# Optimization experiments

Hardware: AMD Instinct MI355X
Metric: run time of the kernel (lower is better)

The kernel has to match this reference:

```python
import jax, jax.numpy as jnp
import numpy as np

N_NODES = 100000
N_EDGES = 1600000
N_GRAPHS = 1000
NODES_PER_GRAPH = 100  # batch vector is arange(N)//100: exactly 100 nodes per graph
HID = 32
MAX_Z = 1000
K = 30
D_LAT = HID * 3 + 1  # 97, total_latent_dim


def setup_inputs() -> dict:
    key = jax.random.key(0)
    ks = jax.random.split(key, 24)
    s = 1.0 / np.sqrt(HID)
    inp = {
        "z": jax.random.randint(ks[0], (N_NODES,), 0, MAX_Z, dtype=jnp.int32),
        "edge_index": jax.random.randint(ks[1], (2, N_EDGES), 0, N_NODES, dtype=jnp.int32),
        "batch": (jnp.arange(N_NODES, dtype=jnp.int32) // NODES_PER_GRAPH),
        "edge_weight": jax.random.uniform(ks[2], (N_EDGES,), jnp.float32, 0.1, 1.0),
        "z_emb": jax.random.normal(ks[3], (MAX_Z, HID), jnp.float32) * 0.1,
        # GCNConv stack: [32->32, 32->32, 32->32, 32->1]
        "Wg1": jax.random.normal(ks[4], (HID, HID)) * s,
        "bg1": jnp.zeros((HID,), jnp.float32),
        "Wg2": jax.random.normal(ks[5], (HID, HID)) * s,
        "bg2": jnp.zeros((HID,), jnp.float32),
        "Wg3": jax.random.normal(ks[6], (HID, HID)) * s,
        "bg3": jnp.zeros((HID,), jnp.float32),
        "Wg4": jax.random.normal(ks[7], (HID, 1)) * s,
        "bg4": jnp.zeros((1,), jnp.float32),
        # Conv1d(1, 16, kernel=97, stride=97)
        "Wc1": jax.random.normal(ks[8], (16, D_LAT)) * (1.0 / np.sqrt(D_LAT)),
        "bc1": jnp.zeros((16,), jnp.float32),
        # Conv1d(16, 32, kernel=5, stride=1)
        "Wc2": jax.random.normal(ks[9], (32, 16, 5)) * (1.0 / np.sqrt(16 * 5)),
        "bc2": jnp.zeros((32,), jnp.float32),
        # Linear(352, 128), Linear(128, 1)
        "Wl1": jax.random.normal(ks[10], (352, 128)) * (1.0 / np.sqrt(352)),
        "bl1": jnp.zeros((128,), jnp.float32),
        "Wl2": jax.random.normal(ks[11], (128, 1)) * (1.0 / np.sqrt(128)),
        "bl2": jnp.zeros((1,), jnp.float32),
    }
    return inp


def gcn_conv(x, src, dst, ew, W, b, n):
    # PyG GCNConv: xW, add self-loops (weight 1), sym-normalize, aggregate at dst, + bias
    xw = x @ W
    deg = jax.ops.segment_sum(ew, dst, num_segments=n) + 1.0  # +1 for self loop
    dinv = jnp.where(deg > 0, jax.lax.rsqrt(deg), 0.0)
    norm = dinv[src] * ew * dinv[dst]                          # [E]
    out = jax.ops.segment_sum(norm[:, None] * xw[src], dst, num_segments=n)
    out = out + xw * (dinv * dinv)[:, None]                    # self-loop term
    return out + b


def _forward(z, edge_index, batch, edge_weight, z_emb, Wg1, bg1, Wg2, bg2, Wg3, bg3,
             Wg4, bg4, Wc1, bc1, Wc2, bc2, Wl1, bl1, Wl2, bl2):
    src, dst = edge_index[0], edge_index[1]
    n = z.shape[0]
    x = z_emb[z]                                              # [N, 32]
    xs = []
    h = x
    for W, b in ((Wg1, bg1), (Wg2, bg2), (Wg3, bg3), (Wg4, bg4)):
        h = jnp.tanh(gcn_conv(h, src, dst, edge_weight, W, b, n))
        xs.append(h)
    x = jnp.concatenate(xs, axis=-1)                          # [N, 97]
    # global_sort_pool: batch is uniform (100 nodes/graph) so dense batching is a reshape
    dense = x.reshape(N_GRAPHS, NODES_PER_GRAPH, D_LAT)       # [B, 100, 97]
    idx = jnp.argsort(-dense[:, :, -1], axis=1)[:, :K]        # sort desc by last channel
    top = jnp.take_along_axis(dense, idx[:, :, None], axis=1)  # [B, 30, 97]
    # Conv1d(1,16,97,stride=97) on flattened [B,1,30*97] == per-slot dense layer
    y = jax.nn.relu(jnp.einsum('bkd,cd->bck', top, Wc1) + bc1[None, :, None])  # [B,16,30]
    y = y.reshape(N_GRAPHS, 16, K // 2, 2).max(axis=-1)        # MaxPool1d(2,2) -> [B,16,15]
    y = jax.lax.conv_general_dilated(y, Wc2, (1,), 'VALID',
                                     dimension_numbers=('NCH', 'OIH', 'NCH'))
    y = jax.nn.relu(y + bc2[None, :, None])                    # [B,32,11]
    y = y.reshape(N_GRAPHS, -1)                                # [B,352]
    y = jax.nn.relu(y @ Wl1 + bl1)                             # dropout: eval mode, identity
    return y @ Wl2 + bl2                                       # [B,1]


def reference(z, edge_index, batch, edge_weight, z_emb, Wg1, bg1, Wg2, bg2, Wg3, bg3,
              Wg4, bg4, Wc1, bc1, Wc2, bc2, Wl1, bl1, Wl2, bl2):
    return _forward(z, edge_index, batch, edge_weight, z_emb, Wg1, bg1, Wg2, bg2, Wg3,
                    bg3, Wg4, bg4, Wc1, bc1, Wc2, bc2, Wl1, bl1, Wl2, bl2)
```

## Files before the change

### kernel.cpp

```cpp
#include <hip/hip_runtime.h>

#define HID 32
#define DLAT 97
#define NPG 100
#define TOPK 30
#define BKT_NODES 128
#define BKT_SHIFT 7
#define MAXBKT 1024
#define CAP 3072
#define CHUNK 8192


__global__ __launch_bounds__(256) void binA_kernel(const int* __restrict__ dst,
                                                   int* __restrict__ bucket_cnt, int E) {
    __shared__ int hist[MAXBKT];
    for (int t = threadIdx.x; t < MAXBKT; t += 256) hist[t] = 0;
    __syncthreads();
    int base = blockIdx.x * CHUNK;
    int lim = min(E, base + CHUNK);
    for (int e = base + threadIdx.x; e < lim; e += 256)
        atomicAdd(&hist[dst[e] >> BKT_SHIFT], 1);
    __syncthreads();
    for (int t = threadIdx.x; t < MAXBKT; t += 256) {
        int v = hist[t];
        if (v) atomicAdd(&bucket_cnt[t], v);
    }
}

__global__ __launch_bounds__(MAXBKT) void bscan_kernel(const int* __restrict__ bucket_cnt,
                                                       int* __restrict__ bucket_start,
                                                       int* __restrict__ cursor) {
    __shared__ int sh[MAXBKT];
    int t = threadIdx.x;
    int v = bucket_cnt[t];
    sh[t] = v;
    __syncthreads();
    for (int off = 1; off < MAXBKT; off <<= 1) {
        int tv = (t >= off) ? sh[t - off] : 0;
        __syncthreads();
        sh[t] += tv;
        __syncthreads();
    }
    int excl = sh[t] - v;
    bucket_start[t] = excl;
    cursor[t] = excl;
    if (t == MAXBKT - 1) bucket_start[MAXBKT] = sh[t];
}

__global__ __launch_bounds__(256) void binB_kernel(const int* __restrict__ src,
                                                   const int* __restrict__ dst,
                                                   const float* __restrict__ ew,
                                                   int* __restrict__ cursor,
                                                   int2* __restrict__ bedge, int E) {
    __shared__ int hist[MAXBKT];
    __shared__ int lcur[MAXBKT];
    __shared__ int dcache[CHUNK];
    for (int t = threadIdx.x; t < MAXBKT; t += 256) hist[t] = 0;
    __syncthreads();
    int base = blockIdx.x * CHUNK;
    int M = min(E - base, CHUNK);
    for (int i = threadIdx.x; i < M; i += 256) {
        int d = dst[base + i];
        dcache[i] = d;
        atomicAdd(&hist[d >> BKT_SHIFT], 1);
    }
    __syncthreads();
    for (int t = threadIdx.x; t < MAXBKT; t += 256) {
        int v = hist[t];
        lcur[t] = v ? atomicAdd(&cursor[t], v) : 0;
    }
    __syncthreads();
    for (int i = threadIdx.x; i < M; i += 256) {
        int d = dcache[i];
        int slot = atomicAdd(&lcur[d >> BKT_SHIFT], 1);
        bedge[slot] = make_int2(src[base + i] | ((d & (BKT_NODES - 1)) << 20),
                                __float_as_int(ew[base + i]));
    }
}

__global__ __launch_bounds__(256) void sortlocal_kernel(
    const int2* __restrict__ bedge, const int* __restrict__ bucket_start,
    int2* __restrict__ csr, int* __restrict__ row_start, float* __restrict__ dinv,
    int N, int E) {
    __shared__ int2 LDSe[CAP];
    __shared__ int cnt[BKT_NODES];
    __shared__ int sh[BKT_NODES];
    __shared__ int lcur[BKT_NODES];
    __shared__ float facc[BKT_NODES];
    int b = blockIdx.x, t = threadIdx.x;
    int beg = bucket_start[b], end = bucket_start[b + 1], M = end - beg;
    if (t < BKT_NODES) { cnt[t] = 0; facc[t] = 0.f; }
    __syncthreads();
    int n = b * BKT_NODES + t;
    if (M <= CAP) {
        for (int i = t; i < M; i += 256) {
            int2 e = bedge[beg + i];
            LDSe[i] = e;
            atomicAdd(&cnt[(e.x >> 20) & (BKT_NODES - 1)], 1);
        }
        __syncthreads();
        int v = 0;
        if (t < BKT_NODES) { v = cnt[t]; sh[t] = v; }
        __syncthreads();
        for (int off = 1; off < BKT_NODES; off <<= 1) {
            int tv = (t >= off && t < BKT_NODES) ? sh[t - off] : 0;
            __syncthreads();
            if (t < BKT_NODES) sh[t] += tv;
            __syncthreads();
        }
        int excl = 0;
        if (t < BKT_NODES) {
            excl = sh[t] - v;
            lcur[t] = excl;
            if (n < N) row_start[n] = beg + excl;
        }
        if (b == 0 && t == 0) row_start[N] = E;
        __syncthreads();
        for (int i = t; i < M; i += 256) {
            int2 e = LDSe[i];
            int slot = atomicAdd(&lcur[(e.x >> 20) & (BKT_NODES - 1)], 1);
            csr[beg + slot] = make_int2(e.x & 0xFFFFF, e.y);
        }
        __syncthreads();
        if (t < BKT_NODES && n < N) {
            float s = 1.f;
            int s0 = beg + excl;
            for (int i = 0; i < v; ++i) s += __int_as_float(csr[s0 + i].y);
            dinv[n] = 1.f / sqrtf(s);
        }
    } else {
        for (int i = beg + t; i < end; i += 256) {
            int2 e = bedge[i];
            int loc = (e.x >> 20) & (BKT_NODES - 1);
            atomicAdd(&cnt[loc], 1);
            atomicAdd(&facc[loc], __int_as_float(e.y));
        }
        __syncthreads();
        int v = 0;
        if (t < BKT_NODES) { v = cnt[t]; sh[t] = v; }
        __syncthreads();
        for (int off = 1; off < BKT_NODES; off <<= 1) {
            int tv = (t >= off && t < BKT_NODES) ? sh[t - off] : 0;
            __syncthreads();
            if (t < BKT_NODES) sh[t] += tv;
            __syncthreads();
        }
        if (t < BKT_NODES) {
            int excl = sh[t] - v;
            lcur[t] = excl;
            if (n < N) {
                row_start[n] = beg + excl;
                dinv[n] = 1.f / sqrtf(1.f + facc[t]);
            }
        }
        if (b == 0 && t == 0) row_start[N] = E;
        __syncthreads();
        for (int i = beg + t; i < end; i += 256) {
            int2 e = bedge[i];
            int slot = atomicAdd(&lcur[(e.x >> 20) & (BKT_NODES - 1)], 1);
            csr[beg + slot] = make_int2(e.x & 0xFFFFF, e.y);
        }
    }
}

__global__ void xw1_kernel(const int* __restrict__ z, const float* __restrict__ z_emb,
                           const float* __restrict__ W, const float* __restrict__ dinv,
                           float* __restrict__ xw, int N) {
    int tid = blockIdx.x * blockDim.x + threadIdx.x;
    if (tid >= N * HID) return;
    int n = tid >> 5, f = tid & 31;
    const float* row = z_emb + (size_t)z[n] * HID;
    float s = 0.f;
#pragma unroll
    for (int k = 0; k < HID; ++k) s += row[k] * W[k * HID + f];
    xw[tid] = s * dinv[n];
}

template <int MODE>
__global__ __launch_bounds__(256) void agg32f_kernel(
    const int* __restrict__ row_start, const int2* __restrict__ csr,
    const float* __restrict__ xw, const float* __restrict__ b,
    const float* __restrict__ dinv, const float* __restrict__ Wn,
    float* __restrict__ concat, int col_off, float* __restrict__ xw_next, int N) {
    int tid = blockIdx.x * blockDim.x + threadIdx.x;
    int n = tid >> 5;
    if (n >= N) return;
    int f = threadIdx.x & 31;
    int beg = row_start[n], end = row_start[n + 1];
    float s0 = 0.f, s1 = 0.f;
    for (int i = beg; i < end; i += 8) {
        float w[8];
        int idx[8];
#pragma unroll
        for (int j = 0; j < 8; ++j) {
            int ii = min(i + j, end - 1);
            int2 v = csr[ii];
            idx[j] = v.x;
            w[j] = (i + j < end) ? __int_as_float(v.y) : 0.f;
        }
        float x[8];
#pragma unroll
        for (int j = 0; j < 8; ++j) x[j] = xw[(size_t)idx[j] * HID + f];
#pragma unroll
        for (int j = 0; j < 8; ++j) {
            if (j & 1) s1 += w[j] * x[j];
            else       s0 += w[j] * x[j];
        }
    }
    float s = s0 + s1;
    float di = dinv[n];
    float outv = tanhf(di * (s + xw[(size_t)n * HID + f]) + b[f]);
    concat[(size_t)n * DLAT + col_off + f] = outv;

    if (MODE == 0) {
        float p = 0.f;
#pragma unroll
        for (int k = 0; k < HID; ++k) {
            float ok = __shfl(outv, k, 32);
            p += ok * Wn[k * HID + f];
        }
        xw_next[(size_t)n * HID + f] = p * di;
    } else {
        float p = outv * Wn[f];
        p += __shfl_xor(p, 16);
        p += __shfl_xor(p, 8);
        p += __shfl_xor(p, 4);
        p += __shfl_xor(p, 2);
        p += __shfl_xor(p, 1);
        if (f == 0) xw_next[n] = p * di;
    }
}

__global__ __launch_bounds__(128) void topk_head_kernel(
    const int* __restrict__ row_start, const int2* __restrict__ csr,
    const float* __restrict__ xw4, const float* __restrict__ b4,
    const float* __restrict__ dinv, const float* __restrict__ concat,
    const float* __restrict__ Wc1, const float* __restrict__ bc1,
    const float* __restrict__ Wc2, const float* __restrict__ bc2,
    const float* __restrict__ Wl1, const float* __restrict__ bl1,
    const float* __restrict__ Wl2, const float* __restrict__ bl2,
    float* __restrict__ out) {
    int g = blockIdx.x;
    int tid = threadIdx.x;
    __shared__ float v[NPG];
    __shared__ int tidx[TOPK];
    __shared__ float tval[TOPK];
    __shared__ float top[TOPK * DLAT];
    __shared__ float y1[16 * TOPK];
    __shared__ float y2[16 * 15];
    __shared__ float y3[352];
    __shared__ float r[128];

    if (tid < NPG) {
        int n = g * NPG + tid;
        int beg = row_start[n], end = row_start[n + 1];
        float s = 0.f;
        for (int i = beg; i < end; ++i) {
            int2 e = csr[i];
            s += __int_as_float(e.y) * xw4[e.x];
        }
        v[tid] = tanhf(dinv[n] * (s + xw4[n]) + b4[0]);
    }
    __syncthreads();
    if (tid < NPG) {
        float vi = v[tid];
        int cnt = 0;
#pragma unroll 4
        for (int j = 0; j < NPG; ++j) {
            float vj = v[j];
            cnt += (vj > vi) || (vj == vi && j < tid);
        }
        if (cnt < TOPK) {
            tidx[cnt] = g * NPG + tid;
            tval[cnt] = vi;
        }
    }
    __syncthreads();

    for (int idx = tid; idx < TOPK * DLAT; idx += 128) {
        int k = idx / DLAT, d = idx - k * DLAT;
        top[idx] = (d == 96) ? tval[k] : concat[(size_t)tidx[k] * DLAT + d];
    }
    __syncthreads();

    for (int idx = tid; idx < 16 * TOPK; idx += 128) {
        int c = idx / TOPK, k = idx % TOPK;
        float s = bc1[c];
        const float* w = Wc1 + c * DLAT;
        const float* t = top + k * DLAT;
#pragma unroll 4
        for (int d = 0; d < DLAT; ++d) s += t[d] * w[d];
        y1[c * TOPK + k] = fmaxf(s, 0.f);
    }
    __syncthreads();

    for (int idx = tid; idx < 16 * 15; idx += 128) {
        int c = idx / 15, j = idx % 15;
        y2[idx] = fmaxf(y1[c * TOPK + 2 * j], y1[c * TOPK + 2 * j + 1]);
    }
    __syncthreads();

    for (int idx = tid; idx < 352; idx += 128) {
        int o = idx / 11, t = idx % 11;
        float s = bc2[o];
#pragma unroll
        for (int i = 0; i < 16; ++i) {
#pragma unroll
            for (int k = 0; k < 5; ++k)
                s += Wc2[(o * 16 + i) * 5 + k] * y2[i * 15 + t + k];
        }
        y3[idx] = fmaxf(s, 0.f);
    }
    __syncthreads();

    {
        float s = bl1[tid];
        for (int d = 0; d < 352; ++d) s += y3[d] * Wl1[d * 128 + tid];
        r[tid] = fmaxf(s, 0.f) * Wl2[tid];
    }
    __syncthreads();
    if (tid < 64) r[tid] += r[tid + 64];
    __syncthreads();
    if (tid == 0) {
        float s = 0.f;
        for (int j = 0; j < 64; ++j) s += r[j];
        out[g] = s + bl2[0];
    }
}


extern "C" void kernel_launch(void* const* d_in, const int* in_sizes, int n_in,
                              void* d_out, int out_size, void* d_ws, size_t ws_size,
                              hipStream_t stream) {
    const int* z = (const int*)d_in[0];
    const int* ei = (const int*)d_in[1];
    const float* ew = (const float*)d_in[3];
    const float* z_emb = (const float*)d_in[4];
    const float* Wg[4] = {(const float*)d_in[5], (const float*)d_in[7],
                          (const float*)d_in[9], (const float*)d_in[11]};
    const float* bg[4] = {(const float*)d_in[6], (const float*)d_in[8],
                          (const float*)d_in[10], (const float*)d_in[12]};
    const float* Wc1 = (const float*)d_in[13];
    const float* bc1 = (const float*)d_in[14];
    const float* Wc2 = (const float*)d_in[15];
    const float* bc2 = (const float*)d_in[16];
    const float* Wl1 = (const float*)d_in[17];
    const float* bl1 = (const float*)d_in[18];
    const float* Wl2 = (const float*)d_in[19];
    const float* bl2 = (const float*)d_in[20];
    float* out = (float*)d_out;

    const int N = in_sizes[0];
    const int E = in_sizes[1] / 2;
    const int G = out_size;
    const int* src = ei;
    const int* dst = ei + E;

    auto cdiv = [](long long a, long long b) { return (int)((a + b - 1) / b); };
    const int NB = cdiv(E, CHUNK);
    const int NBKT = cdiv(N, BKT_NODES);

    char* ws = (char*)d_ws;
    int2* bedge = (int2*)ws;                  ws += sizeof(int2) * (size_t)E;
    int2* csr = (int2*)ws;                    ws += sizeof(int2) * (size_t)E;
    int* bucket_cnt = (int*)ws;               ws += sizeof(int) * MAXBKT;
    int* bucket_start = (int*)ws;             ws += sizeof(int) * (MAXBKT + 1);
    int* cursor = (int*)ws;                   ws += sizeof(int) * MAXBKT;
    int* row_start = (int*)ws;                ws += sizeof(int) * (N + 1);
    float* dinv = (float*)ws;                 ws += sizeof(float) * N;
    float* xw_a = (float*)ws;                 ws += sizeof(float) * (size_t)N * HID;
    float* concat = (float*)ws;               ws += sizeof(float) * (size_t)N * DLAT;
    float* xw4 = (float*)ws;                  ws += sizeof(float) * N;
    float* xw_b = (float*)bedge;

    const int B = 256;

    hipMemsetAsync(bucket_cnt, 0, sizeof(int) * MAXBKT, stream);
    binA_kernel<<<NB, B, 0, stream>>>(dst, bucket_cnt, E);
    bscan_kernel<<<1, MAXBKT, 0, stream>>>(bucket_cnt, bucket_start, cursor);
    binB_kernel<<<NB, B, 0, stream>>>(src, dst, ew, cursor, bedge, E);
    sortlocal_kernel<<<NBKT, B, 0, stream>>>(bedge, bucket_start, csr, row_start,
                                             dinv, N, E);

    xw1_kernel<<<cdiv((long long)N * HID, B), B, 0, stream>>>(z, z_emb, Wg[0], dinv, xw_a, N);
    const int AGGB = cdiv((long long)N * 32, B);
    agg32f_kernel<0><<<AGGB, B, 0, stream>>>(row_start, csr, xw_a, bg[0], dinv, Wg[1],
                                             concat, 0, xw_b, N);
    agg32f_kernel<0><<<AGGB, B, 0, stream>>>(row_start, csr, xw_b, bg[1], dinv, Wg[2],
                                             concat, 32, xw_a, N);
    agg32f_kernel<1><<<AGGB, B, 0, stream>>>(row_start, csr, xw_a, bg[2], dinv, Wg[3],
                                             concat, 64, xw4, N);

    topk_head_kernel<<<G, 128, 0, stream>>>(row_start, csr, xw4, bg[3], dinv, concat,
                                            Wc1, bc1, Wc2, bc2, Wl1, bl1, Wl2, bl2, out);
}
```

Baseline: 417.5 us.

## Precompute per-atom-type embedding×W table and gather it in first aggregation

```diff
diff --git a/kernel.cpp b/kernel.cpp
--- a/kernel.cpp
+++ b/kernel.cpp
@@ -4,6 +4,7 @@
 #define DLAT 97
 #define NPG 100
 #define TOPK 30
+#define MAXZ 1000
 #define BKT_NODES 128
 #define BKT_SHIFT 7
 #define MAXBKT 1024
@@ -80,8 +81,8 @@
 
 __global__ __launch_bounds__(256) void sortlocal_kernel(
     const int2* __restrict__ bedge, const int* __restrict__ bucket_start,
-    int2* __restrict__ csr, int* __restrict__ row_start, float* __restrict__ dinv,
-    int N, int E) {
+    const int* __restrict__ z, int2* __restrict__ csr, int* __restrict__ row_start,
+    float* __restrict__ dinv, int2* __restrict__ ni, int N, int E) {
     __shared__ int2 LDSe[CAP];
     __shared__ int cnt[BKT_NODES];
     __shared__ int sh[BKT_NODES];
@@ -126,7 +127,9 @@
             float s = 1.f;
             int s0 = beg + excl;
             for (int i = 0; i < v; ++i) s += __int_as_float(csr[s0 + i].y);
-            dinv[n] = 1.f / sqrtf(s);
+            float di = 1.f / sqrtf(s);
+            dinv[n] = di;
+            ni[n] = make_int2(z[n], __float_as_int(di));
         }
     } else {
         for (int i = beg + t; i < end; i += 256) {
@@ -150,7 +153,9 @@
             lcur[t] = excl;
             if (n < N) {
                 row_start[n] = beg + excl;
-                dinv[n] = 1.f / sqrtf(1.f + facc[t]);
+                float di = 1.f / sqrtf(1.f + facc[t]);
+                dinv[n] = di;
+                ni[n] = make_int2(z[n], __float_as_int(di));
             }
         }
         if (b == 0 && t == 0) row_start[N] = E;
@@ -163,17 +168,59 @@
     }
 }
 
-__global__ void xw1_kernel(const int* __restrict__ z, const float* __restrict__ z_emb,
-                           const float* __restrict__ W, const float* __restrict__ dinv,
-                           float* __restrict__ xw, int N) {
+__global__ void ztab_kernel(const float* __restrict__ z_emb, const float* __restrict__ W,
+                            float* __restrict__ T) {
     int tid = blockIdx.x * blockDim.x + threadIdx.x;
-    if (tid >= N * HID) return;
-    int n = tid >> 5, f = tid & 31;
-    const float* row = z_emb + (size_t)z[n] * HID;
+    if (tid >= MAXZ * HID) return;
+    int zi = tid >> 5, f = tid & 31;
+    const float* row = z_emb + (size_t)zi * HID;
     float s = 0.f;
 #pragma unroll
     for (int k = 0; k < HID; ++k) s += row[k] * W[k * HID + f];
-    xw[tid] = s * dinv[n];
+    T[tid] = s;
+}
+
+__global__ __launch_bounds__(256) void agg1st_kernel(
+    const int* __restrict__ row_start, const int2* __restrict__ csr,
+    const int2* __restrict__ ni, const float* __restrict__ T,
+    const float* __restrict__ b, const float* __restrict__ Wn,
+    float* __restrict__ concat, float* __restrict__ xw_next, int N) {
+    int tid = blockIdx.x * blockDim.x + threadIdx.x;
+    int n = tid >> 5;
+    if (n >= N) return;
+    int f = threadIdx.x & 31;
+    int beg = row_start[n], end = row_start[n + 1];
+    float s0 = 0.f, s1 = 0.f;
+    for (int i = beg; i < end; i += 8) {
+        int2 e[8];
+#pragma unroll
+        for (int j = 0; j < 8; ++j) e[j] = csr[min(i + j, end - 1)];
+        int2 nio[8];
+#pragma unroll
+        for (int j = 0; j < 8; ++j) nio[j] = ni[e[j].x];
+        float x[8];
+#pragma unroll
+        for (int j = 0; j < 8; ++j) x[j] = T[nio[j].x * HID + f];
+#pragma unroll
+        for (int j = 0; j < 8; ++j) {
+            float w = (i + j < end)
+                          ? __int_as_float(e[j].y) * __int_as_float(nio[j].y) : 0.f;
+            if (j & 1) s1 += w * x[j];
+            else       s0 += w * x[j];
+        }
+    }
+    float s = s0 + s1;
+    int2 me = ni[n];
+    float di = __int_as_float(me.y);
+    float outv = tanhf(di * (s + di * T[me.x * HID + f]) + b[f]);
+    concat[(size_t)n * DLAT + f] = outv;
+    float p = 0.f;
+#pragma unroll
+    for (int k = 0; k < HID; ++k) {
+        float ok = __shfl(outv, k, 32);
+        p += ok * Wn[k * HID + f];
+    }
+    xw_next[(size_t)n * HID + f] = p * di;
 }
 
 template <int MODE>
@@ -363,15 +410,17 @@
     char* ws = (char*)d_ws;
     int2* bedge = (int2*)ws;                  ws += sizeof(int2) * (size_t)E;
     int2* csr = (int2*)ws;                    ws += sizeof(int2) * (size_t)E;
+    int2* ni = (int2*)ws;                     ws += sizeof(int2) * (size_t)N;
     int* bucket_cnt = (int*)ws;               ws += sizeof(int) * MAXBKT;
     int* bucket_start = (int*)ws;             ws += sizeof(int) * (MAXBKT + 1);
     int* cursor = (int*)ws;                   ws += sizeof(int) * MAXBKT;
     int* row_start = (int*)ws;                ws += sizeof(int) * (N + 1);
     float* dinv = (float*)ws;                 ws += sizeof(float) * N;
+    float* T = (float*)ws;                    ws += sizeof(float) * MAXZ * HID;
     float* xw_a = (float*)ws;                 ws += sizeof(float) * (size_t)N * HID;
     float* concat = (float*)ws;               ws += sizeof(float) * (size_t)N * DLAT;
-    float* xw4 = (float*)ws;                  ws += sizeof(float) * N;
     float* xw_b = (float*)bedge;
+    float* xw4 = (float*)ni;
 
     const int B = 256;
 
@@ -379,13 +428,13 @@
     binA_kernel<<<NB, B, 0, stream>>>(dst, bucket_cnt, E);
     bscan_kernel<<<1, MAXBKT, 0, stream>>>(bucket_cnt, bucket_start, cursor);
     binB_kernel<<<NB, B, 0, stream>>>(src, dst, ew, cursor, bedge, E);
-    sortlocal_kernel<<<NBKT, B, 0, stream>>>(bedge, bucket_start, csr, row_start,
-                                             dinv, N, E);
-
-    xw1_kernel<<<cdiv((long long)N * HID, B), B, 0, stream>>>(z, z_emb, Wg[0], dinv, xw_a, N);
+    sortlocal_kernel<<<NBKT, B, 0, stream>>>(bedge, bucket_start, z, csr, row_start,
+                                             dinv, ni, N, E);
+
+    ztab_kernel<<<cdiv(MAXZ * HID, B), B, 0, stream>>>(z_emb, Wg[0], T);
     const int AGGB = cdiv((long long)N * 32, B);
-    agg32f_kernel<0><<<AGGB, B, 0, stream>>>(row_start, csr, xw_a, bg[0], dinv, Wg[1],
-                                             concat, 0, xw_b, N);
+    agg1st_kernel<<<AGGB, B, 0, stream>>>(row_start, csr, ni, T, bg[0], Wg[1],
+                                          concat, xw_b, N);
     agg32f_kernel<0><<<AGGB, B, 0, stream>>>(row_start, csr, xw_b, bg[1], dinv, Wg[2],
                                              concat, 32, xw_a, N);
     agg32f_kernel<1><<<AGGB, B, 0, stream>>>(row_start, csr, xw_a, bg[2], dinv, Wg[3],
```

Result: no change. 423.6 us (+1.5%).

## Fuse CSR build stages and first projection into one cooperative kernel

Applied to the files above, without the earlier changes.

```diff
diff --git a/kernel.cpp b/kernel.cpp
--- a/kernel.cpp
+++ b/kernel.cpp
@@ -1,4 +1,7 @@
 #include <hip/hip_runtime.h>
+#include <hip/hip_cooperative_groups.h>
+
+namespace cg = cooperative_groups;
 
 #define HID 32
 #define DLAT 97
@@ -6,174 +9,166 @@
 #define TOPK 30
 #define BKT_NODES 128
 #define BKT_SHIFT 7
-#define MAXBKT 1024
+#define NBUCK 1024
 #define CAP 3072
 #define CHUNK 8192
 
-
-__global__ __launch_bounds__(256) void binA_kernel(const int* __restrict__ dst,
-                                                   int* __restrict__ bucket_cnt, int E) {
-    __shared__ int hist[MAXBKT];
-    for (int t = threadIdx.x; t < MAXBKT; t += 256) hist[t] = 0;
-    __syncthreads();
-    int base = blockIdx.x * CHUNK;
-    int lim = min(E, base + CHUNK);
-    for (int e = base + threadIdx.x; e < lim; e += 256)
-        atomicAdd(&hist[dst[e] >> BKT_SHIFT], 1);
-    __syncthreads();
-    for (int t = threadIdx.x; t < MAXBKT; t += 256) {
-        int v = hist[t];
-        if (v) atomicAdd(&bucket_cnt[t], v);
-    }
-}
-
-__global__ __launch_bounds__(MAXBKT) void bscan_kernel(const int* __restrict__ bucket_cnt,
-                                                       int* __restrict__ bucket_start,
-                                                       int* __restrict__ cursor) {
-    __shared__ int sh[MAXBKT];
-    int t = threadIdx.x;
-    int v = bucket_cnt[t];
-    sh[t] = v;
-    __syncthreads();
-    for (int off = 1; off < MAXBKT; off <<= 1) {
-        int tv = (t >= off) ? sh[t - off] : 0;
-        __syncthreads();
-        sh[t] += tv;
-        __syncthreads();
-    }
-    int excl = sh[t] - v;
-    bucket_start[t] = excl;
-    cursor[t] = excl;
-    if (t == MAXBKT - 1) bucket_start[MAXBKT] = sh[t];
-}
-
-__global__ __launch_bounds__(256) void binB_kernel(const int* __restrict__ src,
-                                                   const int* __restrict__ dst,
-                                                   const float* __restrict__ ew,
-                                                   int* __restrict__ cursor,
-                                                   int2* __restrict__ bedge, int E) {
-    __shared__ int hist[MAXBKT];
-    __shared__ int lcur[MAXBKT];
+__global__ __launch_bounds__(256) void coopbuild_kernel(
+    const int* __restrict__ src, const int* __restrict__ dst,
+    const float* __restrict__ ew, const int* __restrict__ z,
+    const float* __restrict__ z_emb, const float* __restrict__ W1,
+    int* __restrict__ bucket_cnt, int* __restrict__ cursor_off,
+    int2* __restrict__ bedge, int2* __restrict__ csr, int* __restrict__ row_start,
+    float* __restrict__ dinv, float* __restrict__ xw_a, int N, int E, int NBKT) {
     __shared__ int dcache[CHUNK];
-    for (int t = threadIdx.x; t < MAXBKT; t += 256) hist[t] = 0;
-    __syncthreads();
-    int base = blockIdx.x * CHUNK;
-    int M = min(E - base, CHUNK);
-    for (int i = threadIdx.x; i < M; i += 256) {
+    __shared__ int hist[NBUCK];
+    __shared__ int lcur[NBUCK];
+    __shared__ int bstart[NBUCK + 1];
+    __shared__ int sh256[256];
+    __shared__ float W1L[HID * HID];
+    __shared__ int cnt[BKT_NODES];
+    __shared__ int sh2[BKT_NODES];
+    __shared__ int lc2[BKT_NODES];
+    __shared__ int zloc[BKT_NODES];
+    __shared__ float dloc[BKT_NODES];
+    int2* LDSe = (int2*)dcache;
+
+    cg::grid_group grid = cg::this_grid();
+    const int t = threadIdx.x;
+    const int base = blockIdx.x * CHUNK;
+    const int M = min(E - base, CHUNK);
+
+    for (int i = t; i < NBUCK; i += 256) hist[i] = 0;
+    for (int i = t; i < HID * HID; i += 256) W1L[i] = W1[i];
+    __syncthreads();
+    for (int i = t; i < M; i += 256) {
         int d = dst[base + i];
         dcache[i] = d;
         atomicAdd(&hist[d >> BKT_SHIFT], 1);
     }
     __syncthreads();
-    for (int t = threadIdx.x; t < MAXBKT; t += 256) {
-        int v = hist[t];
-        lcur[t] = v ? atomicAdd(&cursor[t], v) : 0;
-    }
-    __syncthreads();
-    for (int i = threadIdx.x; i < M; i += 256) {
+    for (int i = t; i < NBUCK; i += 256) {
+        int v = hist[i];
+        if (v) atomicAdd(&bucket_cnt[i], v);
+    }
+    grid.sync();
+
+    {
+        int t4 = t * 4;
+        int a0 = bucket_cnt[t4], a1 = bucket_cnt[t4 + 1];
+        int a2 = bucket_cnt[t4 + 2], a3 = bucket_cnt[t4 + 3];
+        int tsum = a0 + a1 + a2 + a3;
+        sh256[t] = tsum;
+        __syncthreads();
+        for (int off = 1; off < 256; off <<= 1) {
+            int tv = (t >= off) ? sh256[t - off] : 0;
+            __syncthreads();
+            sh256[t] += tv;
+            __syncthreads();
+        }
+        int excl = sh256[t] - tsum;
+        bstart[t4] = excl;
+        bstart[t4 + 1] = excl + a0;
+        bstart[t4 + 2] = excl + a0 + a1;
+        bstart[t4 + 3] = excl + a0 + a1 + a2;
+        if (t == 255) bstart[NBUCK] = excl + tsum;
+    }
+    __syncthreads();
+
+    for (int i = t; i < NBUCK; i += 256) {
+        int v = hist[i];
+        lcur[i] = bstart[i] + (v ? atomicAdd(&cursor_off[i], v) : 0);
+    }
+    __syncthreads();
+    for (int i = t; i < M; i += 256) {
         int d = dcache[i];
         int slot = atomicAdd(&lcur[d >> BKT_SHIFT], 1);
         bedge[slot] = make_int2(src[base + i] | ((d & (BKT_NODES - 1)) << 20),
                                 __float_as_int(ew[base + i]));
     }
-}
-
-__global__ __launch_bounds__(256) void sortlocal_kernel(
-    const int2* __restrict__ bedge, const int* __restrict__ bucket_start,
-    int2* __restrict__ csr, int* __restrict__ row_start, float* __restrict__ dinv,
-    int N, int E) {
-    __shared__ int2 LDSe[CAP];
-    __shared__ int cnt[BKT_NODES];
-    __shared__ int sh[BKT_NODES];
-    __shared__ int lcur[BKT_NODES];
-    __shared__ float facc[BKT_NODES];
-    int b = blockIdx.x, t = threadIdx.x;
-    int beg = bucket_start[b], end = bucket_start[b + 1], M = end - beg;
-    if (t < BKT_NODES) { cnt[t] = 0; facc[t] = 0.f; }
-    __syncthreads();
-    int n = b * BKT_NODES + t;
-    if (M <= CAP) {
-        for (int i = t; i < M; i += 256) {
-            int2 e = bedge[beg + i];
-            LDSe[i] = e;
-            atomicAdd(&cnt[(e.x >> 20) & (BKT_NODES - 1)], 1);
-        }
-        __syncthreads();
-        int v = 0;
-        if (t < BKT_NODES) { v = cnt[t]; sh[t] = v; }
-        __syncthreads();
-        for (int off = 1; off < BKT_NODES; off <<= 1) {
-            int tv = (t >= off && t < BKT_NODES) ? sh[t - off] : 0;
-            __syncthreads();
-            if (t < BKT_NODES) sh[t] += tv;
-            __syncthreads();
-        }
-        int excl = 0;
-        if (t < BKT_NODES) {
-            excl = sh[t] - v;
-            lcur[t] = excl;
-            if (n < N) row_start[n] = beg + excl;
-        }
-        if (b == 0 && t == 0) row_start[N] = E;
-        __syncthreads();
-        for (int i = t; i < M; i += 256) {
-            int2 e = LDSe[i];
-            int slot = atomicAdd(&lcur[(e.x >> 20) & (BKT_NODES - 1)], 1);
-            csr[beg + slot] = make_int2(e.x & 0xFFFFF, e.y);
+    grid.sync();
+
+    if (blockIdx.x == 0 && t == 0) row_start[N] = E;
+    for (int b = blockIdx.x; b < NBKT; b += gridDim.x) {
+        int beg = bstart[b], end = bstart[b + 1], Mb = end - beg;
+        if (t < BKT_NODES) cnt[t] = 0;
+        __syncthreads();
+        int v = 0, excl = 0;
+        int n = b * BKT_NODES + t;
+        if (Mb <= CAP) {
+            for (int i = t; i < Mb; i += 256) {
+                int2 e = bedge[beg + i];
+                LDSe[i] = e;
+                atomicAdd(&cnt[(e.x >> 20) & (BKT_NODES - 1)], 1);
+            }
+            __syncthreads();
+            if (t < BKT_NODES) { v = cnt[t]; sh2[t] = v; }
+            __syncthreads();
+            for (int off = 1; off < BKT_NODES; off <<= 1) {
+                int tv = (t >= off && t < BKT_NODES) ? sh2[t - off] : 0;
+                __syncthreads();
+                if (t < BKT_NODES) sh2[t] += tv;
+                __syncthreads();
+            }
+            if (t < BKT_NODES) {
+                excl = sh2[t] - v;
+                lc2[t] = excl;
+                if (n < N) row_start[n] = beg + excl;
+            }
+            __syncthreads();
+            for (int i = t; i < Mb; i += 256) {
+                int2 e = LDSe[i];
+                int slot = atomicAdd(&lc2[(e.x >> 20) & (BKT_NODES - 1)], 1);
+                csr[beg + slot] = make_int2(e.x & 0xFFFFF, e.y);
+            }
+        } else {
+            for (int i = beg + t; i < end; i += 256) {
+                int2 e = bedge[i];
+                atomicAdd(&cnt[(e.x >> 20) & (BKT_NODES - 1)], 1);
+            }
+            __syncthreads();
+            if (t < BKT_NODES) { v = cnt[t]; sh2[t] = v; }
+            __syncthreads();
+            for (int off = 1; off < BKT_NODES; off <<= 1) {
+                int tv = (t >= off && t < BKT_NODES) ? sh2[t - off] : 0;
+                __syncthreads();
+                if (t < BKT_NODES) sh2[t] += tv;
+                __syncthreads();
+            }
+            if (t < BKT_NODES) {
+                excl = sh2[t] - v;
+                lc2[t] = excl;
+                if (n < N) row_start[n] = beg + excl;
+            }
+            __syncthreads();
+            for (int i = beg + t; i < end; i += 256) {
+                int2 e = bedge[i];
+                int slot = atomicAdd(&lc2[(e.x >> 20) & (BKT_NODES - 1)], 1);
+                csr[beg + slot] = make_int2(e.x & 0xFFFFF, e.y);
+            }
         }
         __syncthreads();
         if (t < BKT_NODES && n < N) {
             float s = 1.f;
             int s0 = beg + excl;
             for (int i = 0; i < v; ++i) s += __int_as_float(csr[s0 + i].y);
-            dinv[n] = 1.f / sqrtf(s);
-        }
-    } else {
-        for (int i = beg + t; i < end; i += 256) {
-            int2 e = bedge[i];
-            int loc = (e.x >> 20) & (BKT_NODES - 1);
-            atomicAdd(&cnt[loc], 1);
-            atomicAdd(&facc[loc], __int_as_float(e.y));
-        }
-        __syncthreads();
-        int v = 0;
-        if (t < BKT_NODES) { v = cnt[t]; sh[t] = v; }
-        __syncthreads();
-        for (int off = 1; off < BKT_NODES; off <<= 1) {
-            int tv = (t >= off && t < BKT_NODES) ? sh[t - off] : 0;
-            __syncthreads();
-            if (t < BKT_NODES) sh[t] += tv;
-            __syncthreads();
-        }
-        if (t < BKT_NODES) {
-            int excl = sh[t] - v;
-            lcur[t] = excl;
-            if (n < N) {
-                row_start[n] = beg + excl;
-                dinv[n] = 1.f / sqrtf(1.f + facc[t]);
-            }
-        }
-        if (b == 0 && t == 0) row_start[N] = E;
-        __syncthreads();
-        for (int i = beg + t; i < end; i += 256) {
-            int2 e = bedge[i];
-            int slot = atomicAdd(&lcur[(e.x >> 20) & (BKT_NODES - 1)], 1);
-            csr[beg + slot] = make_int2(e.x & 0xFFFFF, e.y);
-        }
-    }
-}
-
-__global__ void xw1_kernel(const int* __restrict__ z, const float* __restrict__ z_emb,
-                           const float* __restrict__ W, const float* __restrict__ dinv,
-                           float* __restrict__ xw, int N) {
-    int tid = blockIdx.x * blockDim.x + threadIdx.x;
-    if (tid >= N * HID) return;
-    int n = tid >> 5, f = tid & 31;
-    const float* row = z_emb + (size_t)z[n] * HID;
-    float s = 0.f;
-#pragma unroll
-    for (int k = 0; k < HID; ++k) s += row[k] * W[k * HID + f];
-    xw[tid] = s * dinv[n];
+            float di = 1.f / sqrtf(s);
+            dinv[n] = di;
+            dloc[t] = di;
+            zloc[t] = z[n];
+        }
+        __syncthreads();
+        int lim = min(BKT_NODES, N - b * BKT_NODES) * HID;
+        for (int idx = t; idx < lim; idx += 256) {
+            int nl = idx >> 5, f = idx & 31;
+            const float* row = z_emb + (size_t)zloc[nl] * HID;
+            float s = 0.f;
+#pragma unroll
+            for (int k = 0; k < HID; ++k) s += row[k] * W1L[k * HID + f];
+            xw_a[(size_t)(b * BKT_NODES + nl) * HID + f] = s * dloc[nl];
+        }
+        __syncthreads();
+    }
 }
 
 template <int MODE>
@@ -350,22 +345,22 @@
     const float* bl2 = (const float*)d_in[20];
     float* out = (float*)d_out;
 
-    const int N = in_sizes[0];
-    const int E = in_sizes[1] / 2;
+    int N = in_sizes[0];
+    int E = in_sizes[1] / 2;
     const int G = out_size;
     const int* src = ei;
     const int* dst = ei + E;
 
     auto cdiv = [](long long a, long long b) { return (int)((a + b - 1) / b); };
     const int NB = cdiv(E, CHUNK);
-    const int NBKT = cdiv(N, BKT_NODES);
+    int NBKT = cdiv(N, BKT_NODES);
 
     char* ws = (char*)d_ws;
     int2* bedge = (int2*)ws;                  ws += sizeof(int2) * (size_t)E;
     int2* csr = (int2*)ws;                    ws += sizeof(int2) * (size_t)E;
-    int* bucket_cnt = (int*)ws;               ws += sizeof(int) * MAXBKT;
-    int* bucket_start = (int*)ws;             ws += sizeof(int) * (MAXBKT + 1);
-    int* cursor = (int*)ws;                   ws += sizeof(int) * MAXBKT;
+    int* ctrl = (int*)ws;                     ws += sizeof(int) * 2 * NBUCK;
+    int* bucket_cnt = ctrl;
+    int* cursor_off = ctrl + NBUCK;
     int* row_start = (int*)ws;                ws += sizeof(int) * (N + 1);
     float* dinv = (float*)ws;                 ws += sizeof(float) * N;
     float* xw_a = (float*)ws;                 ws += sizeof(float) * (size_t)N * HID;
@@ -375,14 +370,17 @@
 
     const int B = 256;
 
-    hipMemsetAsync(bucket_cnt, 0, sizeof(int) * MAXBKT, stream);
-    binA_kernel<<<NB, B, 0, stream>>>(dst, bucket_cnt, E);
-    bscan_kernel<<<1, MAXBKT, 0, stream>>>(bucket_cnt, bucket_start, cursor);
-    binB_kernel<<<NB, B, 0, stream>>>(src, dst, ew, cursor, bedge, E);
-    sortlocal_kernel<<<NBKT, B, 0, stream>>>(bedge, bucket_start, csr, row_start,
-                                             dinv, N, E);
-
-    xw1_kernel<<<cdiv((long long)N * HID, B), B, 0, stream>>>(z, z_emb, Wg[0], dinv, xw_a, N);
+    hipMemsetAsync(ctrl, 0, sizeof(int) * 2 * NBUCK, stream);
+    {
+        void* args[] = {(void*)&src, (void*)&dst, (void*)&ew, (void*)&z,
+                        (void*)&z_emb, (void*)&Wg[0], (void*)&bucket_cnt,
+                        (void*)&cursor_off, (void*)&bedge, (void*)&csr,
+                        (void*)&row_start, (void*)&dinv, (void*)&xw_a,
+                        (void*)&N, (void*)&E, (void*)&NBKT};
+        hipLaunchCooperativeKernel((void*)coopbuild_kernel, dim3(NB), dim3(B),
+                                   args, 0, stream);
+    }
+
     const int AGGB = cdiv((long long)N * 32, B);
     agg32f_kernel<0><<<AGGB, B, 0, stream>>>(row_start, csr, xw_a, bg[0], dinv, Wg[1],
                                              concat, 0, xw_b, N);
```

New measurement: 499.0 us. 19.5% more time.
